# Performance work log

Measured on AMD Instinct MI355X. Metric: run time of the kernel, lower is better.

## Reference

```python
import jax, jax.numpy as jnp
import numpy as np

B, S, D, H = 2, 4096, 512, 8
HD = D // H


def setup_inputs() -> dict:
    key = jax.random.key(0)
    ks = jax.random.split(key, 11)
    s = 1.0 / np.sqrt(D)
    return {
        "queries": jax.random.normal(ks[0], (B, S, D), jnp.float32),
        "keys": jax.random.normal(ks[1], (B, S, D), jnp.float32),
        "values": jax.random.normal(ks[2], (B, S, D), jnp.float32),
        "Wq": jax.random.normal(ks[3], (D, D), jnp.float32) * s,
        "bq": jnp.zeros((D,), jnp.float32),
        "Wk": jax.random.normal(ks[4], (D, D), jnp.float32) * s,
        "bk": jnp.zeros((D,), jnp.float32),
        "Wv": jax.random.normal(ks[5], (D, D), jnp.float32) * s,
        "bv": jnp.zeros((D,), jnp.float32),
        "Wo": jax.random.normal(ks[6], (D, D), jnp.float32) * s,
        "bo": jnp.zeros((D,), jnp.float32),
    }


def reference(queries, keys, values, Wq, bq, Wk, bk, Wv, bv, Wo, bo):
    b = queries.shape[0]
    # Linear projections (torch Linear: x @ W.T + b; here W stored as [in, out])
    q = (queries @ Wq + bq).reshape(b, -1, H, HD)   # [B, Sq, H, HD]
    k = (keys @ Wk + bk).reshape(b, -1, H, HD)       # [B, Sk, H, HD]
    v = (values @ Wv + bv).reshape(b, -1, H, HD)     # [B, Sk, H, HD]
    logits = jnp.einsum('bqhd,bkhd->bhqk', q, k) / jnp.sqrt(jnp.float32(HD))
    attn = jax.nn.softmax(logits, axis=-1)           # [B, H, Sq, Sk]  (dropout_rate=0 -> identity)
    ctx = jnp.einsum('bhqk,bkhd->bqhd', attn, v).reshape(b, -1, H * HD)
    return ctx @ Wo + bo
```

## Files before the change

kernel.cpp:

```cpp
#include <hip/hip_runtime.h>
#include <hip/hip_bf16.h>

constexpr int B_  = 2;
constexpr int S_  = 4096;
constexpr int D_  = 512;
constexpr int H_  = 8;
constexpr int HD_ = 64;
constexpr int M_  = B_ * S_;

typedef __attribute__((ext_vector_type(8))) short short8;
typedef __attribute__((ext_vector_type(4))) float floatx4;

static __device__ __forceinline__ unsigned short f2bf(float f) {
    union { float f; unsigned u; } v; v.f = f;
    unsigned r = v.u + 0x7fffu + ((v.u >> 16) & 1u);
    return (unsigned short)(r >> 16);
}

static __device__ __forceinline__ unsigned pk2bf(float a, float b) {
#if __has_builtin(__builtin_amdgcn_cvt_pk_bf16_f32)
    typedef __attribute__((ext_vector_type(2))) __bf16 bf16x2_t;
    union { bf16x2_t v; unsigned u; } u;
    u.v = __builtin_amdgcn_cvt_pk_bf16_f32(a, b);
    return u.u;
#else
    return (unsigned)f2bf(a) | ((unsigned)f2bf(b) << 16);
#endif
}

#if __has_builtin(__builtin_amdgcn_exp2f)
#define EXP2(x) __builtin_amdgcn_exp2f(x)
#else
#define EXP2(x) exp2f(x)
#endif

#define QSCALE 0.18033688011110204f

static __device__ __forceinline__ void gl_lds16(const void* g, void* l) {
    typedef __attribute__((address_space(1))) const unsigned GU;
    typedef __attribute__((address_space(3))) unsigned LU;
    __builtin_amdgcn_global_load_lds((GU*)g, (LU*)l, 16, 0, 0);
}

__global__ __launch_bounds__(256) void xcast_kernel(
    const float* __restrict__ Xq, const float* __restrict__ Xk, const float* __restrict__ Xv,
    unsigned short* __restrict__ Y) {
    const int z = blockIdx.z;
    const float* X = z == 0 ? Xq : (z == 1 ? Xk : Xv);
    unsigned short* Yz = Y + (size_t)z * M_ * D_;
    const int n8 = M_ * D_ / 8;
    int i = blockIdx.x * 256 + threadIdx.x;
    const int stride = gridDim.x * 256;
    for (; i < n8; i += stride) {
        float4 a = *(const float4*)&X[(size_t)i * 8];
        float4 b = *(const float4*)&X[(size_t)i * 8 + 4];
        union { short8 s; unsigned u[4]; } p;
        p.u[0] = pk2bf(a.x, a.y); p.u[1] = pk2bf(a.z, a.w);
        p.u[2] = pk2bf(b.x, b.y); p.u[3] = pk2bf(b.z, b.w);
        *(short8*)&Yz[(size_t)i * 8] = p.s;
    }
}

__global__ __launch_bounds__(256) void wtrans_kernel(
    const float* __restrict__ Wq, const float* __restrict__ Wk,
    const float* __restrict__ Wv, const float* __restrict__ Wo,
    unsigned short* __restrict__ Tq, unsigned short* __restrict__ Tk,
    unsigned short* __restrict__ Tv, unsigned short* __restrict__ To) {
    const int z = blockIdx.z;
    const float* W = z == 0 ? Wq : (z == 1 ? Wk : (z == 2 ? Wv : Wo));
    unsigned short* Wt = z == 0 ? Tq : (z == 1 ? Tk : (z == 2 ? Tv : To));
    __shared__ float T[64][65];
    const int t = threadIdx.x;
    const int k0 = blockIdx.x * 64, n0 = blockIdx.y * 64;
#pragma unroll
    for (int i = 0; i < 4; ++i) {
        const int flat = t + 256 * i;
        const int kr = flat >> 4, nc = (flat & 15) * 4;
        float4 v = *(const float4*)&W[(size_t)(k0 + kr) * 512 + n0 + nc];
        T[kr][nc] = v.x; T[kr][nc + 1] = v.y; T[kr][nc + 2] = v.z; T[kr][nc + 3] = v.w;
    }
    __syncthreads();
#pragma unroll
    for (int i = 0; i < 4; ++i) {
        const int flat = t + 256 * i;
        const int nr = flat >> 4, kc = (flat & 15) * 4;
        ushort4 o4;
        o4.x = f2bf(T[kc][nr]);     o4.y = f2bf(T[kc + 1][nr]);
        o4.z = f2bf(T[kc + 2][nr]); o4.w = f2bf(T[kc + 3][nr]);
        *(ushort4*)&Wt[(size_t)(n0 + nr) * 512 + k0 + kc] = o4;
    }
}

template <int MODE>
__global__ __launch_bounds__(256, 3) void gemm_kernel(
    const unsigned short* __restrict__ Ab,
    const unsigned short* __restrict__ Wt,
    const float* __restrict__ b0, const float* __restrict__ b1, const float* __restrict__ b2,
    unsigned short* __restrict__ o0, unsigned short* __restrict__ o1,
    unsigned short* __restrict__ o2, float* __restrict__ of) {
    __shared__ unsigned short As[128 * 64];
    __shared__ unsigned short Bs[128 * 64];

    const int tid  = threadIdx.x;
    const int w    = tid >> 6;
    const int lane = tid & 63;
    const int n0   = blockIdx.x * 128;
    const int m0   = blockIdx.y * 128;
    const int lm   = lane & 15;
    const int lq   = lane >> 4;
    const int wm   = (w >> 1) * 64;
    const int wn   = (w & 1) * 64;

    const int z = MODE == 0 ? (n0 >> 9) : 0;
    const unsigned short* A = MODE == 0 ? Ab + (size_t)z * M_ * D_ : Ab;

    const int srow = lane >> 3;
    const int sch  = lane & 7;
    const int ca   = (sch ^ (srow & 7)) * 8;

    floatx4 acc[4][4];
#pragma unroll
    for (int i = 0; i < 4; ++i)
#pragma unroll
        for (int j = 0; j < 4; ++j) acc[i][j] = (floatx4)0.0f;

    for (int kb = 0; kb < 8; ++kb) {
        const int k0 = kb * 64;
        __syncthreads();
#pragma unroll
        for (int it = 0; it < 4; ++it) {
            const int r8 = w * 32 + it * 8;
            gl_lds16(&A [(size_t)(m0 + r8 + srow) * 512 + k0 + ca], &As[r8 * 64]);
            gl_lds16(&Wt[(size_t)(n0 + r8 + srow) * 512 + k0 + ca], &Bs[r8 * 64]);
        }
        __syncthreads();

        short8 af[2][4], bf[2][4];
#pragma unroll
        for (int ks = 0; ks < 2; ++ks)
#pragma unroll
            for (int i = 0; i < 4; ++i) {
                const int cc = ((ks * 4 + lq) ^ (lm & 7)) * 8;
                af[ks][i] = *(const short8*)&As[(wm + i * 16 + lm) * 64 + cc];
                bf[ks][i] = *(const short8*)&Bs[(wn + i * 16 + lm) * 64 + cc];
            }
#pragma unroll
        for (int ks = 0; ks < 2; ++ks)
#pragma unroll
            for (int mi = 0; mi < 4; ++mi)
#pragma unroll
                for (int ni = 0; ni < 4; ++ni)
                    acc[mi][ni] = __builtin_amdgcn_mfma_f32_16x16x32_bf16(
                        af[ks][mi], bf[ks][ni], acc[mi][ni], 0, 0, 0);
    }

    const float* bias = MODE == 0 ? (z == 0 ? b0 : (z == 1 ? b1 : b2)) : b0;
    const float scale = (MODE == 0 && z == 0) ? QSCALE : 1.0f;
    const int nl0 = n0 & 511;

    float bias_n[4];
#pragma unroll
    for (int ni = 0; ni < 4; ++ni) bias_n[ni] = bias[nl0 + wn + ni * 16 + lm];

#pragma unroll
    for (int mi = 0; mi < 4; ++mi) {
#pragma unroll
        for (int ni = 0; ni < 4; ++ni) {
            if (MODE == 1) {
                const int gn = n0 + wn + ni * 16 + lm;
#pragma unroll
                for (int r = 0; r < 4; ++r) {
                    const int gm = m0 + wm + mi * 16 + lq * 4 + r;
                    of[(size_t)gm * 512 + gn] = acc[mi][ni][r] + bias_n[ni];
                }
            } else {
                const int gnl = nl0 + wn + ni * 16 + lm;
                const int h = gnl >> 6, hd = gnl & 63;
                if (z == 2) {
                    const int gm = m0 + wm + mi * 16 + lq * 4;
                    const int b = gm >> 12, s = gm & 4095;
                    union { ushort4 s4; uint2 u; } o4;
                    o4.u.x = pk2bf(acc[mi][ni][0] + bias_n[ni], acc[mi][ni][1] + bias_n[ni]);
                    o4.u.y = pk2bf(acc[mi][ni][2] + bias_n[ni], acc[mi][ni][3] + bias_n[ni]);
                    *(ushort4*)&o2[(((size_t)(b * 8 + h)) * 64 + hd) * 4096 + s] = o4.s4;
                } else {
                    unsigned short* out = z == 0 ? o0 : o1;
#pragma unroll
                    for (int r = 0; r < 4; ++r) {
                        const int gm = m0 + wm + mi * 16 + lq * 4 + r;
                        const int b = gm >> 12, s = gm & 4095;
                        const float vv = (acc[mi][ni][r] + bias_n[ni]) * scale;
                        out[(((size_t)(b * 8 + h)) * 4096 + s) * 64 + hd] = f2bf(vv);
                    }
                }
            }
        }
    }
}

__global__ __launch_bounds__(256, 2) void flash_kernel(
    const unsigned short* __restrict__ Q, const unsigned short* __restrict__ K,
    const unsigned short* __restrict__ Vt, unsigned short* __restrict__ ctx) {
    __shared__ unsigned short Ks[64 * 64];
    __shared__ unsigned short Vs[64 * 64];
    __shared__ unsigned short Ps[4][16 * 64];

    const int tid = threadIdx.x;
    const int w   = tid >> 6;
    const int l   = tid & 63;
    const int lm  = l & 15;
    const int lq  = l >> 4;
    const int q0  = blockIdx.x * 128;
    const int bh  = blockIdx.y;

    const size_t base = (size_t)bh * S_ * HD_;
    const unsigned short* Qg = Q + base;
    const unsigned short* Kg = K + base;
    const unsigned short* Vg = Vt + base;

    short8 qf[2][2];
#pragma unroll
    for (int qn = 0; qn < 2; ++qn) {
        const unsigned short* qp = &Qg[(size_t)(q0 + w * 32 + qn * 16 + lm) * 64];
        qf[qn][0] = *(const short8*)(qp + lq * 8);
        qf[qn][1] = *(const short8*)(qp + 32 + lq * 8);
    }

    short8 ones;
#pragma unroll
    for (int j = 0; j < 8; ++j) ones[j] = (short)0x3F80;

    floatx4 o[2][4];
#pragma unroll
    for (int qn = 0; qn < 2; ++qn)
#pragma unroll
        for (int i = 0; i < 4; ++i) o[qn][i] = (floatx4)0.0f;
    floatx4 ls[2];
    ls[0] = (floatx4)0.0f; ls[1] = (floatx4)0.0f;

    const int sr  = tid >> 3, sch = tid & 7;
    const int sw0 = sr * 64 + ((sch ^ (sr & 7)) * 8);
    const int sw1 = (sr + 32) * 64 + ((sch ^ (sr & 7)) * 8);
    const int lm7 = lm & 7;

    short8 kr0, kr1, vr0, vr1;
    kr0 = *(const short8*)&Kg[(size_t)sr * 64 + sch * 8];
    kr1 = *(const short8*)&Kg[(size_t)(sr + 32) * 64 + sch * 8];
    vr0 = *(const short8*)&Vg[(size_t)sr * S_ + sch * 8];
    vr1 = *(const short8*)&Vg[(size_t)(sr + 32) * S_ + sch * 8];

    for (int kt = 0; kt < 64; ++kt) {
        __syncthreads();
        *(short8*)&Ks[sw0] = kr0;
        *(short8*)&Ks[sw1] = kr1;
        *(short8*)&Vs[sw0] = vr0;
        *(short8*)&Vs[sw1] = vr1;
        __syncthreads();
        if (kt < 63) {
            const int t1 = (kt + 1) * 64;
            kr0 = *(const short8*)&Kg[(size_t)(t1 + sr) * 64 + sch * 8];
            kr1 = *(const short8*)&Kg[(size_t)(t1 + sr + 32) * 64 + sch * 8];
            vr0 = *(const short8*)&Vg[(size_t)sr * S_ + t1 + sch * 8];
            vr1 = *(const short8*)&Vg[(size_t)(sr + 32) * S_ + t1 + sch * 8];
        }

        short8 kf[2][4];
#pragma unroll
        for (int ks = 0; ks < 2; ++ks)
#pragma unroll
            for (int ni = 0; ni < 4; ++ni)
                kf[ks][ni] = *(const short8*)&Ks[(ni * 16 + lm) * 64 +
                                                 (((ks * 4 + lq) ^ lm7) * 8)];

        floatx4 sf[2][4];
#pragma unroll
        for (int qn = 0; qn < 2; ++qn)
#pragma unroll
            for (int ni = 0; ni < 4; ++ni) sf[qn][ni] = (floatx4)0.0f;
#pragma unroll
        for (int ks = 0; ks < 2; ++ks)
#pragma unroll
            for (int qn = 0; qn < 2; ++qn)
#pragma unroll
                for (int ni = 0; ni < 4; ++ni)
                    sf[qn][ni] = __builtin_amdgcn_mfma_f32_16x16x32_bf16(
                        kf[ks][ni], qf[qn][ks], sf[qn][ni], 0, 0, 0);

        short8 vf[2][4];
#pragma unroll
        for (int c = 0; c < 2; ++c)
#pragma unroll
            for (int ni = 0; ni < 4; ++ni)
                vf[c][ni] = *(const short8*)&Vs[(ni * 16 + lm) * 64 +
                                                (((c * 4 + lq) ^ lm7) * 8)];

        unsigned short* Pw = &Ps[w][0];
#pragma unroll
        for (int qn = 0; qn < 2; ++qn) {
#pragma unroll
            for (int ni = 0; ni < 4; ++ni) {
                uint2 pv;
                pv.x = pk2bf(EXP2(sf[qn][ni][0]), EXP2(sf[qn][ni][1]));
                pv.y = pk2bf(EXP2(sf[qn][ni][2]), EXP2(sf[qn][ni][3]));
                *(uint2*)&Pw[lm * 64 + (((ni * 2 + (lq >> 1)) ^ lm7) * 8) + (lq & 1) * 4] = pv;
            }
#pragma unroll
            for (int c = 0; c < 2; ++c) {
                short8 pf = *(const short8*)&Pw[lm * 64 + (((c * 4 + lq) ^ lm7) * 8)];
                ls[qn] = __builtin_amdgcn_mfma_f32_16x16x32_bf16(ones, pf, ls[qn], 0, 0, 0);
#pragma unroll
                for (int ni = 0; ni < 4; ++ni)
                    o[qn][ni] = __builtin_amdgcn_mfma_f32_16x16x32_bf16(
                        vf[c][ni], pf, o[qn][ni], 0, 0, 0);
            }
        }
    }

    const int b = bh >> 3, h = bh & 7;
#pragma unroll
    for (int qn = 0; qn < 2; ++qn) {
        const float inv = 1.0f / ls[qn][0];
        const int q = q0 + w * 32 + qn * 16 + lm;
        const size_t rb = ((size_t)(b * S_ + q)) * 512 + h * 64;
#pragma unroll
        for (int ni = 0; ni < 4; ++ni) {
            union { ushort4 s; uint2 u; } o4;
            o4.u.x = pk2bf(o[qn][ni][0] * inv, o[qn][ni][1] * inv);
            o4.u.y = pk2bf(o[qn][ni][2] * inv, o[qn][ni][3] * inv);
            *(ushort4*)&ctx[rb + ni * 16 + lq * 4] = o4.s;
        }
    }
}

extern "C" void kernel_launch(void* const* d_in, const int* in_sizes, int n_in,
                              void* d_out, int out_size, void* d_ws, size_t ws_size,
                              hipStream_t stream) {
    const float* queries = (const float*)d_in[0];
    const float* keys    = (const float*)d_in[1];
    const float* values  = (const float*)d_in[2];
    const float* Wq = (const float*)d_in[3];
    const float* bq = (const float*)d_in[4];
    const float* Wk = (const float*)d_in[5];
    const float* bk = (const float*)d_in[6];
    const float* Wv = (const float*)d_in[7];
    const float* bv = (const float*)d_in[8];
    const float* Wo = (const float*)d_in[9];
    const float* bo = (const float*)d_in[10];

    unsigned short* xb    = (unsigned short*)d_ws;
    unsigned short* wsctx = xb;
    unsigned short* wsq   = xb   + (size_t)3 * M_ * D_;
    unsigned short* wsk   = wsq  + (size_t)M_ * D_;
    unsigned short* wsvt  = wsk  + (size_t)M_ * D_;
    unsigned short* wtq   = wsvt + (size_t)M_ * D_;
    unsigned short* wtk   = wtq  + (size_t)D_ * D_;
    unsigned short* wtv   = wtk  + (size_t)D_ * D_;
    unsigned short* wto   = wtv  + (size_t)D_ * D_;

    xcast_kernel<<<dim3(1024, 1, 3), dim3(256), 0, stream>>>(queries, keys, values, xb);
    wtrans_kernel<<<dim3(8, 8, 4), dim3(256), 0, stream>>>(
        Wq, Wk, Wv, Wo, wtq, wtk, wtv, wto);

    gemm_kernel<0><<<dim3(12, 64), dim3(256), 0, stream>>>(
        xb, wtq, bq, bk, bv, wsq, wsk, wsvt, nullptr);

    flash_kernel<<<dim3(S_ / 128, B_ * H_), dim3(256), 0, stream>>>(wsq, wsk, wsvt, wsctx);

    gemm_kernel<1><<<dim3(4, 64), dim3(256), 0, stream>>>(
        wsctx, wto, bo, nullptr, nullptr, nullptr, nullptr, nullptr, (float*)d_out);
}
```

Measured before the change: 243.8 us.

## Fuse fp32-to-bf16 cast into QKV GEMM and restructure flash attention

```diff
diff --git a/kernel.cpp b/kernel.cpp
--- a/kernel.cpp
+++ b/kernel.cpp
@@ -9,6 +9,7 @@
 constexpr int M_  = B_ * S_;
 
 typedef __attribute__((ext_vector_type(8))) short short8;
+typedef __attribute__((ext_vector_type(4))) short short4v;
 typedef __attribute__((ext_vector_type(4))) float floatx4;
 
 static __device__ __forceinline__ unsigned short f2bf(float f) {
@@ -34,31 +35,24 @@
 #define EXP2(x) exp2f(x)
 #endif
 
+#if __has_builtin(__builtin_amdgcn_mfma_f32_16x16x16bf16_1k)
+static __device__ __forceinline__ floatx4 mfma16k(short4v a, short4v b, floatx4 c) {
+    return __builtin_amdgcn_mfma_f32_16x16x16bf16_1k(a, b, c, 0, 0, 0);
+}
+#else
+static __device__ __forceinline__ floatx4 mfma16k(short4v a, short4v b, floatx4 c) {
+    short8 a8 = {a[0], a[1], a[2], a[3], 0, 0, 0, 0};
+    short8 b8 = {b[0], b[1], b[2], b[3], 0, 0, 0, 0};
+    return __builtin_amdgcn_mfma_f32_16x16x32_bf16(a8, b8, c, 0, 0, 0);
+}
+#endif
+
 #define QSCALE 0.18033688011110204f
 
 static __device__ __forceinline__ void gl_lds16(const void* g, void* l) {
     typedef __attribute__((address_space(1))) const unsigned GU;
     typedef __attribute__((address_space(3))) unsigned LU;
     __builtin_amdgcn_global_load_lds((GU*)g, (LU*)l, 16, 0, 0);
-}
-
-__global__ __launch_bounds__(256) void xcast_kernel(
-    const float* __restrict__ Xq, const float* __restrict__ Xk, const float* __restrict__ Xv,
-    unsigned short* __restrict__ Y) {
-    const int z = blockIdx.z;
-    const float* X = z == 0 ? Xq : (z == 1 ? Xk : Xv);
-    unsigned short* Yz = Y + (size_t)z * M_ * D_;
-    const int n8 = M_ * D_ / 8;
-    int i = blockIdx.x * 256 + threadIdx.x;
-    const int stride = gridDim.x * 256;
-    for (; i < n8; i += stride) {
-        float4 a = *(const float4*)&X[(size_t)i * 8];
-        float4 b = *(const float4*)&X[(size_t)i * 8 + 4];
-        union { short8 s; unsigned u[4]; } p;
-        p.u[0] = pk2bf(a.x, a.y); p.u[1] = pk2bf(a.z, a.w);
-        p.u[2] = pk2bf(b.x, b.y); p.u[3] = pk2bf(b.z, b.w);
-        *(short8*)&Yz[(size_t)i * 8] = p.s;
-    }
 }
 
 __global__ __launch_bounds__(256) void wtrans_kernel(
@@ -91,13 +85,122 @@
     }
 }
 
-template <int MODE>
-__global__ __launch_bounds__(256, 3) void gemm_kernel(
-    const unsigned short* __restrict__ Ab,
+__global__ __launch_bounds__(256, 3) void qkv_gemm(
+    const float* __restrict__ Xq, const float* __restrict__ Xk, const float* __restrict__ Xv,
     const unsigned short* __restrict__ Wt,
-    const float* __restrict__ b0, const float* __restrict__ b1, const float* __restrict__ b2,
-    unsigned short* __restrict__ o0, unsigned short* __restrict__ o1,
-    unsigned short* __restrict__ o2, float* __restrict__ of) {
+    const float* __restrict__ bq, const float* __restrict__ bk, const float* __restrict__ bv,
+    unsigned short* __restrict__ Oq, unsigned short* __restrict__ Ok,
+    unsigned short* __restrict__ Ovt) {
+    __shared__ unsigned short As[128 * 64];
+    __shared__ unsigned short Bs[128 * 64];
+
+    const int tid  = threadIdx.x;
+    const int w    = tid >> 6;
+    const int lane = tid & 63;
+    const int bx   = blockIdx.x;
+    const int z    = bx >> 2;
+    const int n0   = bx * 128;
+    const int m0   = blockIdx.y * 128;
+    const int lm   = lane & 15;
+    const int lq   = lane >> 4;
+    const int lm7  = lm & 7;
+    const int wm   = (w >> 1) * 64;
+    const int wn   = (w & 1) * 64;
+
+    const float* A = z == 0 ? Xq : (z == 1 ? Xk : Xv);
+
+    const int arow = w * 32 + (lane >> 1);
+    const int ah   = (lane & 1) * 32;
+    const int srow = lane >> 3;
+    const int slc  = ((lane & 7) ^ (srow & 7)) * 8;
+
+    floatx4 acc[4][4];
+#pragma unroll
+    for (int i = 0; i < 4; ++i)
+#pragma unroll
+        for (int j = 0; j < 4; ++j) acc[i][j] = (floatx4)0.0f;
+
+    for (int kb = 0; kb < 8; ++kb) {
+        const int k0 = kb * 64;
+        __syncthreads();
+        float4 av[8];
+#pragma unroll
+        for (int i = 0; i < 8; ++i)
+            av[i] = *(const float4*)&A[(size_t)(m0 + arow) * 512 + k0 + ah + i * 4];
+#pragma unroll
+        for (int it = 0; it < 4; ++it) {
+            const int r8 = w * 32 + it * 8;
+            gl_lds16(&Wt[(size_t)(n0 + r8 + srow) * 512 + k0 + slc], &Bs[r8 * 64]);
+        }
+#pragma unroll
+        for (int j = 0; j < 4; ++j) {
+            union { short8 s; unsigned u[4]; } p;
+            p.u[0] = pk2bf(av[2 * j].x, av[2 * j].y);
+            p.u[1] = pk2bf(av[2 * j].z, av[2 * j].w);
+            p.u[2] = pk2bf(av[2 * j + 1].x, av[2 * j + 1].y);
+            p.u[3] = pk2bf(av[2 * j + 1].z, av[2 * j + 1].w);
+            const int phys = (((lane & 1) * 4 + j) ^ (arow & 7));
+            *(short8*)&As[arow * 64 + phys * 8] = p.s;
+        }
+        __syncthreads();
+
+        short8 af[2][4], bf[2][4];
+#pragma unroll
+        for (int ks = 0; ks < 2; ++ks)
+#pragma unroll
+            for (int i = 0; i < 4; ++i) {
+                const int cc = ((ks * 4 + lq) ^ lm7) * 8;
+                af[ks][i] = *(const short8*)&As[(wm + i * 16 + lm) * 64 + cc];
+                bf[ks][i] = *(const short8*)&Bs[(wn + i * 16 + lm) * 64 + cc];
+            }
+#pragma unroll
+        for (int ks = 0; ks < 2; ++ks)
+#pragma unroll
+            for (int mi = 0; mi < 4; ++mi)
+#pragma unroll
+                for (int ni = 0; ni < 4; ++ni)
+                    acc[mi][ni] = __builtin_amdgcn_mfma_f32_16x16x32_bf16(
+                        af[ks][mi], bf[ks][ni], acc[mi][ni], 0, 0, 0);
+    }
+
+    const float* bias = z == 0 ? bq : (z == 1 ? bk : bv);
+    const float scale = z == 0 ? QSCALE : 1.0f;
+    const int nl0 = n0 & 511;
+
+    float bias_n[4];
+#pragma unroll
+    for (int ni = 0; ni < 4; ++ni) bias_n[ni] = bias[nl0 + wn + ni * 16 + lm];
+
+#pragma unroll
+    for (int mi = 0; mi < 4; ++mi) {
+#pragma unroll
+        for (int ni = 0; ni < 4; ++ni) {
+            const int gnl = nl0 + wn + ni * 16 + lm;
+            const int h = gnl >> 6, hd = gnl & 63;
+            if (z == 2) {
+                const int gm = m0 + wm + mi * 16 + lq * 4;
+                const int b = gm >> 12, s = gm & 4095;
+                union { ushort4 s4; uint2 u; } o4;
+                o4.u.x = pk2bf(acc[mi][ni][0] + bias_n[ni], acc[mi][ni][1] + bias_n[ni]);
+                o4.u.y = pk2bf(acc[mi][ni][2] + bias_n[ni], acc[mi][ni][3] + bias_n[ni]);
+                *(ushort4*)&Ovt[(((size_t)(b * 8 + h)) * 64 + hd) * 4096 + s] = o4.s4;
+            } else {
+                unsigned short* out = z == 0 ? Oq : Ok;
+#pragma unroll
+                for (int r = 0; r < 4; ++r) {
+                    const int gm = m0 + wm + mi * 16 + lq * 4 + r;
+                    const int b = gm >> 12, s = gm & 4095;
+                    const float vv = (acc[mi][ni][r] + bias_n[ni]) * scale;
+                    out[(((size_t)(b * 8 + h)) * 4096 + s) * 64 + hd] = f2bf(vv);
+                }
+            }
+        }
+    }
+}
+
+__global__ __launch_bounds__(256, 3) void o_gemm(
+    const unsigned short* __restrict__ A, const unsigned short* __restrict__ Wt,
+    const float* __restrict__ bias, float* __restrict__ outp) {
     __shared__ unsigned short As[128 * 64];
     __shared__ unsigned short Bs[128 * 64];
 
@@ -108,15 +211,12 @@
     const int m0   = blockIdx.y * 128;
     const int lm   = lane & 15;
     const int lq   = lane >> 4;
+    const int lm7  = lm & 7;
     const int wm   = (w >> 1) * 64;
     const int wn   = (w & 1) * 64;
 
-    const int z = MODE == 0 ? (n0 >> 9) : 0;
-    const unsigned short* A = MODE == 0 ? Ab + (size_t)z * M_ * D_ : Ab;
-
     const int srow = lane >> 3;
-    const int sch  = lane & 7;
-    const int ca   = (sch ^ (srow & 7)) * 8;
+    const int slc  = ((lane & 7) ^ (srow & 7)) * 8;
 
     floatx4 acc[4][4];
 #pragma unroll
@@ -130,8 +230,8 @@
 #pragma unroll
         for (int it = 0; it < 4; ++it) {
             const int r8 = w * 32 + it * 8;
-            gl_lds16(&A [(size_t)(m0 + r8 + srow) * 512 + k0 + ca], &As[r8 * 64]);
-            gl_lds16(&Wt[(size_t)(n0 + r8 + srow) * 512 + k0 + ca], &Bs[r8 * 64]);
+            gl_lds16(&A [(size_t)(m0 + r8 + srow) * 512 + k0 + slc], &As[r8 * 64]);
+            gl_lds16(&Wt[(size_t)(n0 + r8 + srow) * 512 + k0 + slc], &Bs[r8 * 64]);
         }
         __syncthreads();
 
@@ -140,7 +240,7 @@
         for (int ks = 0; ks < 2; ++ks)
 #pragma unroll
             for (int i = 0; i < 4; ++i) {
-                const int cc = ((ks * 4 + lq) ^ (lm & 7)) * 8;
+                const int cc = ((ks * 4 + lq) ^ lm7) * 8;
                 af[ks][i] = *(const short8*)&As[(wm + i * 16 + lm) * 64 + cc];
                 bf[ks][i] = *(const short8*)&Bs[(wn + i * 16 + lm) * 64 + cc];
             }
@@ -154,62 +254,35 @@
                         af[ks][mi], bf[ks][ni], acc[mi][ni], 0, 0, 0);
     }
 
-    const float* bias = MODE == 0 ? (z == 0 ? b0 : (z == 1 ? b1 : b2)) : b0;
-    const float scale = (MODE == 0 && z == 0) ? QSCALE : 1.0f;
-    const int nl0 = n0 & 511;
-
     float bias_n[4];
 #pragma unroll
-    for (int ni = 0; ni < 4; ++ni) bias_n[ni] = bias[nl0 + wn + ni * 16 + lm];
-
-#pragma unroll
-    for (int mi = 0; mi < 4; ++mi) {
+    for (int ni = 0; ni < 4; ++ni) bias_n[ni] = bias[n0 + wn + ni * 16 + lm];
+
+#pragma unroll
+    for (int mi = 0; mi < 4; ++mi)
 #pragma unroll
         for (int ni = 0; ni < 4; ++ni) {
-            if (MODE == 1) {
-                const int gn = n0 + wn + ni * 16 + lm;
-#pragma unroll
-                for (int r = 0; r < 4; ++r) {
-                    const int gm = m0 + wm + mi * 16 + lq * 4 + r;
-                    of[(size_t)gm * 512 + gn] = acc[mi][ni][r] + bias_n[ni];
-                }
-            } else {
-                const int gnl = nl0 + wn + ni * 16 + lm;
-                const int h = gnl >> 6, hd = gnl & 63;
-                if (z == 2) {
-                    const int gm = m0 + wm + mi * 16 + lq * 4;
-                    const int b = gm >> 12, s = gm & 4095;
-                    union { ushort4 s4; uint2 u; } o4;
-                    o4.u.x = pk2bf(acc[mi][ni][0] + bias_n[ni], acc[mi][ni][1] + bias_n[ni]);
-                    o4.u.y = pk2bf(acc[mi][ni][2] + bias_n[ni], acc[mi][ni][3] + bias_n[ni]);
-                    *(ushort4*)&o2[(((size_t)(b * 8 + h)) * 64 + hd) * 4096 + s] = o4.s4;
-                } else {
-                    unsigned short* out = z == 0 ? o0 : o1;
-#pragma unroll
-                    for (int r = 0; r < 4; ++r) {
-                        const int gm = m0 + wm + mi * 16 + lq * 4 + r;
-                        const int b = gm >> 12, s = gm & 4095;
-                        const float vv = (acc[mi][ni][r] + bias_n[ni]) * scale;
-                        out[(((size_t)(b * 8 + h)) * 4096 + s) * 64 + hd] = f2bf(vv);
-                    }
-                }
-            }
-        }
-    }
-}
-
-__global__ __launch_bounds__(256, 2) void flash_kernel(
+            const int gn = n0 + wn + ni * 16 + lm;
+#pragma unroll
+            for (int r = 0; r < 4; ++r) {
+                const int gm = m0 + wm + mi * 16 + lq * 4 + r;
+                outp[(size_t)gm * 512 + gn] = acc[mi][ni][r] + bias_n[ni];
+            }
+        }
+}
+
+__global__ __launch_bounds__(128) void flash_kernel(
     const unsigned short* __restrict__ Q, const unsigned short* __restrict__ K,
     const unsigned short* __restrict__ Vt, unsigned short* __restrict__ ctx) {
-    __shared__ unsigned short Ks[64 * 64];
-    __shared__ unsigned short Vs[64 * 64];
-    __shared__ unsigned short Ps[4][16 * 64];
+    __shared__ unsigned short Ks[2][64 * 64];
+    __shared__ unsigned short Vs[2][64 * 64];
 
     const int tid = threadIdx.x;
     const int w   = tid >> 6;
     const int l   = tid & 63;
     const int lm  = l & 15;
     const int lq  = l >> 4;
+    const int lm7 = lm & 7;
     const int q0  = blockIdx.x * 128;
     const int bh  = blockIdx.y;
 
@@ -218,116 +291,107 @@
     const unsigned short* Kg = K + base;
     const unsigned short* Vg = Vt + base;
 
-    short8 qf[2][2];
-#pragma unroll
-    for (int qn = 0; qn < 2; ++qn) {
-        const unsigned short* qp = &Qg[(size_t)(q0 + w * 32 + qn * 16 + lm) * 64];
+    short8 qf[4][2];
+#pragma unroll
+    for (int qn = 0; qn < 4; ++qn) {
+        const unsigned short* qp = &Qg[(size_t)(q0 + w * 64 + qn * 16 + lm) * 64];
         qf[qn][0] = *(const short8*)(qp + lq * 8);
         qf[qn][1] = *(const short8*)(qp + 32 + lq * 8);
     }
 
-    short8 ones;
-#pragma unroll
-    for (int j = 0; j < 8; ++j) ones[j] = (short)0x3F80;
-
-    floatx4 o[2][4];
-#pragma unroll
-    for (int qn = 0; qn < 2; ++qn)
+    short4v ones4;
+#pragma unroll
+    for (int j = 0; j < 4; ++j) ones4[j] = (short)0x3F80;
+
+    floatx4 o[4][4];
+#pragma unroll
+    for (int qn = 0; qn < 4; ++qn)
 #pragma unroll
         for (int i = 0; i < 4; ++i) o[qn][i] = (floatx4)0.0f;
-    floatx4 ls[2];
-    ls[0] = (floatx4)0.0f; ls[1] = (floatx4)0.0f;
-
-    const int sr  = tid >> 3, sch = tid & 7;
-    const int sw0 = sr * 64 + ((sch ^ (sr & 7)) * 8);
-    const int sw1 = (sr + 32) * 64 + ((sch ^ (sr & 7)) * 8);
-    const int lm7 = lm & 7;
-
-    short8 kr0, kr1, vr0, vr1;
-    kr0 = *(const short8*)&Kg[(size_t)sr * 64 + sch * 8];
-    kr1 = *(const short8*)&Kg[(size_t)(sr + 32) * 64 + sch * 8];
-    vr0 = *(const short8*)&Vg[(size_t)sr * S_ + sch * 8];
-    vr1 = *(const short8*)&Vg[(size_t)(sr + 32) * S_ + sch * 8];
+    floatx4 ls[4];
+#pragma unroll
+    for (int qn = 0; qn < 4; ++qn) ls[qn] = (floatx4)0.0f;
+
+    const int srow = l >> 3;
+    const int slc  = ((l & 7) ^ (srow & 7)) * 8;
+
+#define STAGE(T0, BUF)                                                           \
+    {                                                                            \
+        _Pragma("unroll") for (int it = 0; it < 4; ++it) {                       \
+            const int r8 = w * 32 + it * 8;                                      \
+            gl_lds16(&Kg[(size_t)((T0) + r8 + srow) * 64 + slc],                 \
+                     &Ks[BUF][r8 * 64]);                                         \
+            gl_lds16(&Vg[(size_t)(r8 + srow) * 4096 + (T0) + slc],               \
+                     &Vs[BUF][r8 * 64]);                                         \
+        }                                                                        \
+    }
+
+    STAGE(0, 0);
+    __syncthreads();
 
     for (int kt = 0; kt < 64; ++kt) {
+        const int cur = kt & 1;
+        if (kt < 63) STAGE((kt + 1) * 64, cur ^ 1);
+
+        short8 kf[2][4];
+#pragma unroll
+        for (int ks = 0; ks < 2; ++ks)
+#pragma unroll
+            for (int ni = 0; ni < 4; ++ni)
+                kf[ks][ni] = *(const short8*)&Ks[cur][(ni * 16 + lm) * 64 +
+                                                      (((ks * 4 + lq) ^ lm7) * 8)];
+        short4v vfr[4][4];
+#pragma unroll
+        for (int mt = 0; mt < 4; ++mt)
+#pragma unroll
+            for (int ni = 0; ni < 4; ++ni)
+                vfr[mt][ni] = *(const short4v*)&Vs[cur][(mt * 16 + lm) * 64 +
+                                                        (((ni * 2 + (lq >> 1)) ^ lm7) * 8) +
+                                                        (lq & 1) * 4];
+
+#pragma unroll
+        for (int qn = 0; qn < 4; ++qn) {
+            floatx4 sf[4];
+#pragma unroll
+            for (int ni = 0; ni < 4; ++ni) sf[ni] = (floatx4)0.0f;
+#pragma unroll
+            for (int ks = 0; ks < 2; ++ks)
+#pragma unroll
+                for (int ni = 0; ni < 4; ++ni)
+                    sf[ni] = __builtin_amdgcn_mfma_f32_16x16x32_bf16(
+                        kf[ks][ni], qf[qn][ks], sf[ni], 0, 0, 0);
+
+            short4v pp[4];
+#pragma unroll
+            for (int ni = 0; ni < 4; ++ni) {
+                union { short4v s; unsigned u[2]; } t;
+                t.u[0] = pk2bf(EXP2(sf[ni][0]), EXP2(sf[ni][1]));
+                t.u[1] = pk2bf(EXP2(sf[ni][2]), EXP2(sf[ni][3]));
+                pp[ni] = t.s;
+            }
+#pragma unroll
+            for (int ni = 0; ni < 4; ++ni) {
+                ls[qn] = mfma16k(ones4, pp[ni], ls[qn]);
+#pragma unroll
+                for (int mt = 0; mt < 4; ++mt)
+                    o[qn][mt] = mfma16k(vfr[mt][ni], pp[ni], o[qn][mt]);
+            }
+        }
         __syncthreads();
-        *(short8*)&Ks[sw0] = kr0;
-        *(short8*)&Ks[sw1] = kr1;
-        *(short8*)&Vs[sw0] = vr0;
-        *(short8*)&Vs[sw1] = vr1;
-        __syncthreads();
-        if (kt < 63) {
-            const int t1 = (kt + 1) * 64;
-            kr0 = *(const short8*)&Kg[(size_t)(t1 + sr) * 64 + sch * 8];
-            kr1 = *(const short8*)&Kg[(size_t)(t1 + sr + 32) * 64 + sch * 8];
-            vr0 = *(const short8*)&Vg[(size_t)sr * S_ + t1 + sch * 8];
-            vr1 = *(const short8*)&Vg[(size_t)(sr + 32) * S_ + t1 + sch * 8];
-        }
-
-        short8 kf[2][4];
-#pragma unroll
-        for (int ks = 0; ks < 2; ++ks)
-#pragma unroll
-            for (int ni = 0; ni < 4; ++ni)
-                kf[ks][ni] = *(const short8*)&Ks[(ni * 16 + lm) * 64 +
-                                                 (((ks * 4 + lq) ^ lm7) * 8)];
-
-        floatx4 sf[2][4];
-#pragma unroll
-        for (int qn = 0; qn < 2; ++qn)
-#pragma unroll
-            for (int ni = 0; ni < 4; ++ni) sf[qn][ni] = (floatx4)0.0f;
-#pragma unroll
-        for (int ks = 0; ks < 2; ++ks)
-#pragma unroll
-            for (int qn = 0; qn < 2; ++qn)
-#pragma unroll
-                for (int ni = 0; ni < 4; ++ni)
-                    sf[qn][ni] = __builtin_amdgcn_mfma_f32_16x16x32_bf16(
-                        kf[ks][ni], qf[qn][ks], sf[qn][ni], 0, 0, 0);
-
-        short8 vf[2][4];
-#pragma unroll
-        for (int c = 0; c < 2; ++c)
-#pragma unroll
-            for (int ni = 0; ni < 4; ++ni)
-                vf[c][ni] = *(const short8*)&Vs[(ni * 16 + lm) * 64 +
-                                                (((c * 4 + lq) ^ lm7) * 8)];
-
-        unsigned short* Pw = &Ps[w][0];
-#pragma unroll
-        for (int qn = 0; qn < 2; ++qn) {
-#pragma unroll
-            for (int ni = 0; ni < 4; ++ni) {
-                uint2 pv;
-                pv.x = pk2bf(EXP2(sf[qn][ni][0]), EXP2(sf[qn][ni][1]));
-                pv.y = pk2bf(EXP2(sf[qn][ni][2]), EXP2(sf[qn][ni][3]));
-                *(uint2*)&Pw[lm * 64 + (((ni * 2 + (lq >> 1)) ^ lm7) * 8) + (lq & 1) * 4] = pv;
-            }
-#pragma unroll
-            for (int c = 0; c < 2; ++c) {
-                short8 pf = *(const short8*)&Pw[lm * 64 + (((c * 4 + lq) ^ lm7) * 8)];
-                ls[qn] = __builtin_amdgcn_mfma_f32_16x16x32_bf16(ones, pf, ls[qn], 0, 0, 0);
-#pragma unroll
-                for (int ni = 0; ni < 4; ++ni)
-                    o[qn][ni] = __builtin_amdgcn_mfma_f32_16x16x32_bf16(
-                        vf[c][ni], pf, o[qn][ni], 0, 0, 0);
-            }
-        }
     }
 
     const int b = bh >> 3, h = bh & 7;
 #pragma unroll
-    for (int qn = 0; qn < 2; ++qn) {
+    for (int qn = 0; qn < 4; ++qn) {
         const float inv = 1.0f / ls[qn][0];
-        const int q = q0 + w * 32 + qn * 16 + lm;
+        const int q = q0 + w * 64 + qn * 16 + lm;
         const size_t rb = ((size_t)(b * S_ + q)) * 512 + h * 64;
 #pragma unroll
-        for (int ni = 0; ni < 4; ++ni) {
+        for (int mt = 0; mt < 4; ++mt) {
             union { ushort4 s; uint2 u; } o4;
-            o4.u.x = pk2bf(o[qn][ni][0] * inv, o[qn][ni][1] * inv);
-            o4.u.y = pk2bf(o[qn][ni][2] * inv, o[qn][ni][3] * inv);
-            *(ushort4*)&ctx[rb + ni * 16 + lq * 4] = o4.s;
+            o4.u.x = pk2bf(o[qn][mt][0] * inv, o[qn][mt][1] * inv);
+            o4.u.y = pk2bf(o[qn][mt][2] * inv, o[qn][mt][3] * inv);
+            *(ushort4*)&ctx[rb + mt * 16 + lq * 4] = o4.s;
         }
     }
 }
@@ -347,25 +411,23 @@
     const float* Wo = (const float*)d_in[9];
     const float* bo = (const float*)d_in[10];
 
-    unsigned short* xb    = (unsigned short*)d_ws;
-    unsigned short* wsctx = xb;
-    unsigned short* wsq   = xb   + (size_t)3 * M_ * D_;
-    unsigned short* wsk   = wsq  + (size_t)M_ * D_;
-    unsigned short* wsvt  = wsk  + (size_t)M_ * D_;
-    unsigned short* wtq   = wsvt + (size_t)M_ * D_;
-    unsigned short* wtk   = wtq  + (size_t)D_ * D_;
-    unsigned short* wtv   = wtk  + (size_t)D_ * D_;
-    unsigned short* wto   = wtv  + (size_t)D_ * D_;
-
-    xcast_kernel<<<dim3(1024, 1, 3), dim3(256), 0, stream>>>(queries, keys, values, xb);
+    unsigned short* wsq   = (unsigned short*)d_ws;
+    unsigned short* wsk   = wsq   + (size_t)M_ * D_;
+    unsigned short* wsvt  = wsk   + (size_t)M_ * D_;
+    unsigned short* wsctx = wsvt  + (size_t)M_ * D_;
+    unsigned short* wtq   = wsctx + (size_t)M_ * D_;
+    unsigned short* wtk   = wtq   + (size_t)D_ * D_;
+    unsigned short* wtv   = wtk   + (size_t)D_ * D_;
+    unsigned short* wto   = wtv   + (size_t)D_ * D_;
+
     wtrans_kernel<<<dim3(8, 8, 4), dim3(256), 0, stream>>>(
         Wq, Wk, Wv, Wo, wtq, wtk, wtv, wto);
 
-    gemm_kernel<0><<<dim3(12, 64), dim3(256), 0, stream>>>(
-        xb, wtq, bq, bk, bv, wsq, wsk, wsvt, nullptr);
-
-    flash_kernel<<<dim3(S_ / 128, B_ * H_), dim3(256), 0, stream>>>(wsq, wsk, wsvt, wsctx);
-
-    gemm_kernel<1><<<dim3(4, 64), dim3(256), 0, stream>>>(
-        wsctx, wto, bo, nullptr, nullptr, nullptr, nullptr, nullptr, (float*)d_out);
-}
+    qkv_gemm<<<dim3(12, 64), dim3(256), 0, stream>>>(
+        queries, keys, values, wtq, bq, bk, bv, wsq, wsk, wsvt);
+
+    flash_kernel<<<dim3(S_ / 128, B_ * H_), dim3(128), 0, stream>>>(
+        wsq, wsk, wsvt, wsctx);
+
+    o_gemm<<<dim3(4, 64), dim3(256), 0, stream>>>(wsctx, wto, bo, (float*)d_out);
+}
```

Result: slower. 311.1 us (+27.6%).
